# Performance work log

Measured on AMD Instinct MI355X. Metric: run time of the kernel, lower is better.

## Reference

```python
import jax, jax.numpy as jnp
import numpy as np
import math

N_EMBED = 1024
N_HEAD = 16
BLOCK_SIZE = 2048

def setup_inputs() -> dict:
    key = jax.random.key(0)
    k1, k2, k3, k4, k5 = jax.random.split(key, 5)
    s = 0.02
    x = jax.random.normal(k1, (2, 2048, N_EMBED), dtype=jnp.float32)
    W_qkv = jax.random.normal(k2, (N_EMBED, 3 * N_EMBED), dtype=jnp.float32) * s
    b_qkv = jax.random.normal(k3, (3 * N_EMBED,), dtype=jnp.float32) * s
    W_out = jax.random.normal(k4, (N_EMBED, N_EMBED), dtype=jnp.float32) * s
    b_out = jax.random.normal(k5, (N_EMBED,), dtype=jnp.float32) * s
    return {"x": x, "W_qkv": W_qkv, "b_qkv": b_qkv, "W_out": W_out, "b_out": b_out}

def reference(x, W_qkv, b_qkv, W_out, b_out):
    b, s, d = x.shape
    hd = d // N_HEAD  # head dim
    qkv = x @ W_qkv + b_qkv                       # [b, s, 3d]
    q, k, v = jnp.split(qkv, 3, axis=-1)
    # [b, h, s, hd]
    q = q.reshape(b, s, N_HEAD, hd).transpose(0, 2, 1, 3)
    k = k.reshape(b, s, N_HEAD, hd).transpose(0, 2, 1, 3)
    v = v.reshape(b, s, N_HEAD, hd).transpose(0, 2, 1, 3)
    scale = 1.0 / math.sqrt(hd)
    sims = jnp.einsum('bhqd,bhkd->bhqk', q, k) * scale  # [b, h, s, s]
    causal = jnp.tril(jnp.ones((s, s), dtype=bool))
    sims = jnp.where(causal[None, None], sims, -jnp.inf)
    probs = jax.nn.softmax(sims, axis=-1)
    attn = jnp.einsum('bhqk,bhkd->bhqd', probs, v)       # [b, h, s, hd]
    attn = attn.transpose(0, 2, 1, 3).reshape(b, s, d)
    return attn @ W_out + b_out
```

## Files before the change

kernel.cpp:

```cpp
#include <hip/hip_runtime.h>
#include <hip/hip_bf16.h>

typedef __attribute__((ext_vector_type(8))) short short8;
typedef __attribute__((ext_vector_type(4))) short short4v;
typedef __attribute__((ext_vector_type(4))) float f32x4;
typedef __attribute__((ext_vector_type(16))) float f32x16;
typedef __attribute__((ext_vector_type(4))) unsigned int u32x4;
typedef unsigned short u16;

__device__ __forceinline__ u16 f2bf(float f) {
  __hip_bfloat16 h = __float2bfloat16(f);
  return __builtin_bit_cast(unsigned short, h);
}

__device__ __forceinline__ unsigned pack2(float lo, float hi) {
  return (unsigned)f2bf(lo) | ((unsigned)f2bf(hi) << 16);
}

__device__ __forceinline__ void gload16(const u16* g, u16* l) {
  __builtin_amdgcn_global_load_lds(
      (const __attribute__((address_space(1))) unsigned int*)g,
      (__attribute__((address_space(3))) unsigned int*)l, 16, 0, 0);
}

__global__ void prep_kernel(const float* __restrict__ x,
                            const float* __restrict__ Wqkv,
                            const float* __restrict__ Wout,
                            u16* __restrict__ Xb,
                            u16* __restrict__ WqkvT,
                            u16* __restrict__ WoutT) {
  __shared__ float tile[32][33];
  const int b = blockIdx.x, tid = threadIdx.x;
  if (b < 4096) {
    const int i = (b * 256 + tid) * 4;
    float4 f = *(const float4*)(x + i);
    uint2 pk;
    pk.x = pack2(f.x, f.y);
    pk.y = pack2(f.z, f.w);
    *(uint2*)(Xb + i) = pk;
    return;
  }
  const float* in;
  u16* out;
  int N, bx, by;
  if (b < 7168) {
    in = Wqkv; out = WqkvT; N = 3072;
    const int bb = b - 4096;
    bx = bb % 96; by = bb / 96;
  } else {
    in = Wout; out = WoutT; N = 1024;
    const int bb = b - 7168;
    bx = bb % 32; by = bb / 32;
  }
  const int n0 = bx * 32, k0 = by * 32;
  const int tx = tid & 31, ty = tid >> 5;
#pragma unroll
  for (int r = 0; r < 4; ++r) {
    const int k = ty + r * 8;
    tile[k][tx] = in[(size_t)(k0 + k) * N + n0 + tx];
  }
  __syncthreads();
#pragma unroll
  for (int r = 0; r < 4; ++r) {
    const int n = ty + r * 8;
    out[(size_t)(n0 + n) * 1024 + k0 + tx] = f2bf(tile[tx][n]);
  }
}

template <int EPI, int BN>
__global__ __launch_bounds__(256, 2) void gemm_kernel(const u16* __restrict__ A,
                                                      const u16* __restrict__ Bt,
                                                      const float* __restrict__ bias,
                                                      void* __restrict__ outp) {
  __shared__ u16 Al[128 * 64];
  __shared__ u16 Bl[BN * 64];
  constexpr int NF = BN / 32;
  const int tid = threadIdx.x;
  const int lane = tid & 63, wid = tid >> 6;
  const int l15 = lane & 15, lg = lane >> 4;
  const int wm = wid >> 1, wn = wid & 1;
  const int m0 = blockIdx.y * 128, n0 = blockIdx.x * BN;

  f32x4 acc[4][NF] = {};

  for (int k0 = 0; k0 < 1024; k0 += 64) {
    __syncthreads();
#pragma unroll
    for (int i = 0; i < 4; ++i) {
      const int p = i * 4096 + tid * 16;
      const int row = p >> 7;
      const int lslot = ((p >> 4) & 7) ^ (row & 7);
      gload16(A + (size_t)(m0 + row) * 1024 + k0 + lslot * 8, Al + i * 2048 + wid * 512);
    }
#pragma unroll
    for (int i = 0; i < NF; ++i) {
      const int p = i * 4096 + tid * 16;
      const int row = p >> 7;
      const int lslot = ((p >> 4) & 7) ^ (row & 7);
      gload16(Bt + (size_t)(n0 + row) * 1024 + k0 + lslot * 8, Bl + i * 2048 + wid * 512);
    }
    __syncthreads();
#pragma unroll
    for (int ks = 0; ks < 2; ++ks) {
      short8 af[4], bfr[NF];
#pragma unroll
      for (int m = 0; m < 4; ++m) {
        const int row = wm * 64 + m * 16 + l15;
        af[m] = *(const short8*)((const char*)Al + row * 128 + (((ks * 4 + lg) ^ (row & 7)) << 4));
      }
#pragma unroll
      for (int n = 0; n < NF; ++n) {
        const int row = wn * (BN / 2) + n * 16 + l15;
        bfr[n] = *(const short8*)((const char*)Bl + row * 128 + (((ks * 4 + lg) ^ (row & 7)) << 4));
      }
#pragma unroll
      for (int m = 0; m < 4; ++m)
#pragma unroll
        for (int n = 0; n < NF; ++n)
          acc[m][n] = __builtin_amdgcn_mfma_f32_16x16x32_bf16(af[m], bfr[n], acc[m][n], 0, 0, 0);
    }
  }

  if (EPI == 0) {
    u16* qkv = (u16*)outp;
#pragma unroll
    for (int m = 0; m < 4; ++m)
#pragma unroll
      for (int n = 0; n < NF; ++n) {
        const int gcol = n0 + wn * (BN / 2) + n * 16 + l15;
        const int which = gcol >> 10, dd = gcol & 1023;
        const int h = dd >> 6, hd = dd & 63;
        const float bb = bias[gcol];
        const int grow0 = m0 + wm * 64 + m * 16 + lg * 4;
        const int b = grow0 >> 11, s0 = grow0 & 2047;
        if (which == 2) {
          const int bsub = (s0 >> 2) & 3;
          const int bper = (bsub == 1) ? 2 : (bsub == 2) ? 1 : bsub;
          const int s0p = (s0 & ~15) | (bper << 2);
          short4v pk;
#pragma unroll
          for (int j = 0; j < 4; ++j) pk[j] = (short)f2bf(acc[m][n][j] + bb);
          *(short4v*)(qkv + (size_t)2 * 4194304 + ((size_t)(b * 16 + h) * 64 + hd) * 2048 + s0p) = pk;
        } else {
          const float sc = (which == 0) ? 0.18033688011112042f : 1.0f;
#pragma unroll
          for (int j = 0; j < 4; ++j) {
            float v = (acc[m][n][j] + bb) * sc;
            qkv[(size_t)which * 4194304 + ((size_t)(b * 16 + h) * 2048 + s0 + j) * 64 + hd] = f2bf(v);
          }
        }
      }
  } else {
    float* O = (float*)outp;
#pragma unroll
    for (int m = 0; m < 4; ++m)
#pragma unroll
      for (int n = 0; n < NF; ++n) {
        const int gcol = n0 + wn * (BN / 2) + n * 16 + l15;
        const float bb = bias[gcol];
#pragma unroll
        for (int j = 0; j < 4; ++j) {
          const int grow = m0 + wm * 64 + m * 16 + lg * 4 + j;
          O[(size_t)grow * 1024 + gcol] = acc[m][n][j] + bb;
        }
      }
  }
}

__global__ __launch_bounds__(512, 4) void attn_kernel(const u16* __restrict__ Q,
                                                      const u16* __restrict__ K,
                                                      const u16* __restrict__ VT,
                                                      u16* __restrict__ Aout) {
  const int bh = blockIdx.y;
  const int p = blockIdx.x;
  const int tid = threadIdx.x, lane = tid & 63, wid = tid >> 6;
  const int l31 = lane & 31, h = lane >> 5;
  const int tl = wid >> 2, qs = (wid >> 1) & 1, kp = wid & 1;

  __shared__ __align__(16) char smem[36864];
  u16(*Kl)[4096] = (u16(*)[4096])smem;
  u16(*Vl)[4096] = (u16(*)[4096])(smem + 16384);

  const u16* Qb = Q + (size_t)bh * 2048 * 64;
  const u16* Kb = K + (size_t)bh * 2048 * 64;
  const u16* Vb = VT + (size_t)bh * 64 * 2048;

  const int tile = tl ? p : (31 - p);
  const int q0 = tile * 64 + qs * 32;
  const int R = 32 - p;

  short8 qf[4];
#pragma unroll
  for (int ks = 0; ks < 4; ++ks)
    qf[ks] = *(const short8*)(Qb + (size_t)(q0 + l31) * 64 + ks * 16 + h * 8);

  short8 ones;
#pragma unroll
  for (int j = 0; j < 8; ++j) ones[j] = (short)0x3F80;

  f32x16 acc[2] = {};
  f32x16 acc_l = {};

  const int srow = tid >> 3;
  const int ssc = ((tid & 7) ^ (srow & 7)) * 8;
  auto stage = [&](int buf, size_t kb) {
    gload16(Kb + (kb + srow) * 64 + ssc, &Kl[buf][wid * 512]);
    gload16(Vb + (size_t)srow * 2048 + kb + ssc, &Vl[buf][wid * 512]);
  };

  stage(0, 0);
  __syncthreads();

  for (int t = 0; t < R; ++t) {
    const int cur = t & 1;
    if (t + 1 < R) stage(cur ^ 1, (size_t)(t + 1) * 64);

    const int kvbase = t * 64 + kp * 32;
    if (kvbase <= q0 + 31) {
      short8 kf[4], vf[2][2];
      const int krow = kp * 32 + l31;
#pragma unroll
      for (int ks = 0; ks < 4; ++ks)
        kf[ks] = *(const short8*)((const char*)&Kl[cur][0] + krow * 128 +
                                  (((ks * 2 + h) ^ (krow & 7)) << 4));
#pragma unroll
      for (int n = 0; n < 2; ++n)
#pragma unroll
        for (int ks = 0; ks < 2; ++ks) {
          const int row = n * 32 + l31;
          vf[n][ks] = *(const short8*)((const char*)&Vl[cur][0] + row * 128 +
                                       (((kp * 4 + ks * 2 + h) ^ (row & 7)) << 4));
        }

      f32x16 sa = {};
      __builtin_amdgcn_s_setprio(1);
#pragma unroll
      for (int ks = 0; ks < 4; ++ks)
        sa = __builtin_amdgcn_mfma_f32_32x32x16_bf16(kf[ks], qf[ks], sa, 0, 0, 0);
      __builtin_amdgcn_s_setprio(0);

      if (kvbase == q0) {
#pragma unroll
        for (int r = 0; r < 16; ++r) {
          const int kvr = (r & 3) + 8 * (r >> 2) + 4 * h;
          if (kvr > l31) sa[r] = -1e30f;
        }
      }
#pragma unroll
      for (int r = 0; r < 16; ++r) sa[r] = exp2f(sa[r]);
      unsigned c[8];
#pragma unroll
      for (int i = 0; i < 8; ++i) c[i] = pack2(sa[2 * i], sa[2 * i + 1]);
      const short8 pk0 = __builtin_bit_cast(short8, (u32x4){c[0], c[1], c[2], c[3]});
      const short8 pk1 = __builtin_bit_cast(short8, (u32x4){c[4], c[5], c[6], c[7]});
      __builtin_amdgcn_s_setprio(1);
      acc_l = __builtin_amdgcn_mfma_f32_32x32x16_bf16(ones, pk0, acc_l, 0, 0, 0);
      acc_l = __builtin_amdgcn_mfma_f32_32x32x16_bf16(ones, pk1, acc_l, 0, 0, 0);
#pragma unroll
      for (int n = 0; n < 2; ++n) {
        acc[n] = __builtin_amdgcn_mfma_f32_32x32x16_bf16(vf[n][0], pk0, acc[n], 0, 0, 0);
        acc[n] = __builtin_amdgcn_mfma_f32_32x32x16_bf16(vf[n][1], pk1, acc[n], 0, 0, 0);
      }
      __builtin_amdgcn_s_setprio(0);
    }
    __syncthreads();
  }

  float* pp = (float*)smem + (((tl << 1) | qs) * 64 + lane) * 36;
  if (kp == 1) {
    pp[0] = acc_l[0];
#pragma unroll
    for (int n = 0; n < 2; ++n)
#pragma unroll
      for (int r = 0; r < 16; ++r) pp[2 + n * 16 + r] = acc[n][r];
  }
  __syncthreads();
  if (kp == 0) {
    const int b = bh >> 4, hh = bh & 15;
    const float inv = 1.0f / (acc_l[0] + pp[0]);
    u16* rowp = Aout + (size_t)(b * 2048 + q0 + l31) * 1024 + hh * 64;
#pragma unroll
    for (int n = 0; n < 2; ++n)
#pragma unroll
      for (int r = 0; r < 16; r += 2) {
        const int hd = n * 32 + (r & 3) + 8 * (r >> 2) + 4 * h;
        const float v0 = (acc[n][r] + pp[2 + n * 16 + r]) * inv;
        const float v1 = (acc[n][r + 1] + pp[2 + n * 16 + r + 1]) * inv;
        *(unsigned*)(rowp + hd) = pack2(v0, v1);
      }
  }
}

extern "C" void kernel_launch(void* const* d_in, const int* in_sizes, int n_in,
                              void* d_out, int out_size, void* d_ws, size_t ws_size,
                              hipStream_t stream) {
  const float* x = (const float*)d_in[0];
  const float* Wqkv = (const float*)d_in[1];
  const float* bqkv = (const float*)d_in[2];
  const float* Wout = (const float*)d_in[3];
  const float* bout = (const float*)d_in[4];

  char* ws = (char*)d_ws;
  u16* Xb = (u16*)(ws + 0);
  u16* WqkvT = (u16*)(ws + 8388608);
  u16* WoutT = (u16*)(ws + 14680064);
  u16* QKV = (u16*)(ws + 16777216);
  u16* Attn = Xb;

  prep_kernel<<<8192, 256, 0, stream>>>(x, Wqkv, Wout, Xb, WqkvT, WoutT);
  gemm_kernel<0, 192><<<dim3(16, 32), 256, 0, stream>>>(Xb, WqkvT, bqkv, QKV);
  attn_kernel<<<dim3(16, 32), 512, 0, stream>>>(QKV, QKV + 4194304, QKV + 8388608, Attn);
  gemm_kernel<1, 64><<<dim3(16, 32), 256, 0, stream>>>(Attn, WoutT, bout, d_out);
}
```

Before: 98.16 us.

## Double-buffer GEMM LDS tiles and use partial vmcnt waits in attention

The GEMM kernel now keeps two LDS buffers for A and B and issues the next K-tile's global-to-LDS loads before computing on the current tile. A partial s_waitcnt vmcnt followed by a raw s_barrier replaces the two full __syncthreads per iteration. The attention loop gets the same change: it waits only for the current tile's loads, not the prefetch. This should hide global load latency behind the MFMA work, but it doubles GEMM LDS use, which may reduce occupancy at two blocks per CU, and correctness depends on the hand-counted vmcnt values.

```diff
diff --git a/kernel.cpp b/kernel.cpp
--- a/kernel.cpp
+++ b/kernel.cpp
@@ -72,9 +72,9 @@
                                                       const u16* __restrict__ Bt,
                                                       const float* __restrict__ bias,
                                                       void* __restrict__ outp) {
-  __shared__ u16 Al[128 * 64];
-  __shared__ u16 Bl[BN * 64];
   constexpr int NF = BN / 32;
+  __shared__ u16 Al[2][128 * 64];
+  __shared__ u16 Bl[2][BN * 64];
   const int tid = threadIdx.x;
   const int lane = tid & 63, wid = tid >> 6;
   const int l15 = lane & 15, lg = lane >> 4;
@@ -83,35 +83,47 @@
 
   f32x4 acc[4][NF] = {};
 
-  for (int k0 = 0; k0 < 1024; k0 += 64) {
-    __syncthreads();
+  auto stageAB = [&](int buf, int k0) {
 #pragma unroll
     for (int i = 0; i < 4; ++i) {
       const int p = i * 4096 + tid * 16;
       const int row = p >> 7;
       const int lslot = ((p >> 4) & 7) ^ (row & 7);
-      gload16(A + (size_t)(m0 + row) * 1024 + k0 + lslot * 8, Al + i * 2048 + wid * 512);
+      gload16(A + (size_t)(m0 + row) * 1024 + k0 + lslot * 8, &Al[buf][i * 2048 + wid * 512]);
     }
 #pragma unroll
     for (int i = 0; i < NF; ++i) {
       const int p = i * 4096 + tid * 16;
       const int row = p >> 7;
       const int lslot = ((p >> 4) & 7) ^ (row & 7);
-      gload16(Bt + (size_t)(n0 + row) * 1024 + k0 + lslot * 8, Bl + i * 2048 + wid * 512);
-    }
-    __syncthreads();
+      gload16(Bt + (size_t)(n0 + row) * 1024 + k0 + lslot * 8, &Bl[buf][i * 2048 + wid * 512]);
+    }
+  };
+
+  stageAB(0, 0);
+
+  for (int k0 = 0; k0 < 1024; k0 += 64) {
+    const int cur = (k0 >> 6) & 1;
+    if (k0 + 64 < 1024) {
+      stageAB(cur ^ 1, k0 + 64);
+      asm volatile("s_waitcnt vmcnt(%0)" ::"n"(4 + NF) : "memory");
+    } else {
+      asm volatile("s_waitcnt vmcnt(0)" ::: "memory");
+    }
+    __builtin_amdgcn_s_barrier();
+    __builtin_amdgcn_sched_barrier(0);
 #pragma unroll
     for (int ks = 0; ks < 2; ++ks) {
       short8 af[4], bfr[NF];
 #pragma unroll
       for (int m = 0; m < 4; ++m) {
         const int row = wm * 64 + m * 16 + l15;
-        af[m] = *(const short8*)((const char*)Al + row * 128 + (((ks * 4 + lg) ^ (row & 7)) << 4));
+        af[m] = *(const short8*)((const char*)&Al[cur][0] + row * 128 + (((ks * 4 + lg) ^ (row & 7)) << 4));
       }
 #pragma unroll
       for (int n = 0; n < NF; ++n) {
         const int row = wn * (BN / 2) + n * 16 + l15;
-        bfr[n] = *(const short8*)((const char*)Bl + row * 128 + (((ks * 4 + lg) ^ (row & 7)) << 4));
+        bfr[n] = *(const short8*)((const char*)&Bl[cur][0] + row * 128 + (((ks * 4 + lg) ^ (row & 7)) << 4));
       }
 #pragma unroll
       for (int m = 0; m < 4; ++m)
@@ -119,6 +131,8 @@
         for (int n = 0; n < NF; ++n)
           acc[m][n] = __builtin_amdgcn_mfma_f32_16x16x32_bf16(af[m], bfr[n], acc[m][n], 0, 0, 0);
     }
+    __builtin_amdgcn_sched_barrier(0);
+    __builtin_amdgcn_s_barrier();
   }
 
   if (EPI == 0) {
@@ -209,11 +223,17 @@
   };
 
   stage(0, 0);
-  __syncthreads();
 
   for (int t = 0; t < R; ++t) {
     const int cur = t & 1;
-    if (t + 1 < R) stage(cur ^ 1, (size_t)(t + 1) * 64);
+    if (t + 1 < R) {
+      stage(cur ^ 1, (size_t)(t + 1) * 64);
+      asm volatile("s_waitcnt vmcnt(2)" ::: "memory");
+    } else {
+      asm volatile("s_waitcnt vmcnt(0)" ::: "memory");
+    }
+    __builtin_amdgcn_s_barrier();
+    __builtin_amdgcn_sched_barrier(0);
 
     const int kvbase = t * 64 + kp * 32;
     if (kvbase <= q0 + 31) {
@@ -263,9 +283,11 @@
       }
       __builtin_amdgcn_s_setprio(0);
     }
-    __syncthreads();
-  }
-
+    __builtin_amdgcn_sched_barrier(0);
+    __builtin_amdgcn_s_barrier();
+  }
+
+  __syncthreads();
   float* pp = (float*)smem + (((tl << 1) | qs) * 64 + lane) * 36;
   if (kp == 1) {
     pp[0] = acc_l[0];
```

Result: slower. 101.1 us (+3.0%).
